# Kernel optimization log

Measured on AMD Instinct MI355X. Metric: run time of the kernel, lower is better.

## Reference

```python
import jax, jax.numpy as jnp
import numpy as np
from jax.scipy.special import logsumexp

# Circuit configuration (matches init_kwargs)
V, K, C = 256, 32, 256        # num_vars, input nodes per var, num categories
N = V * K                     # nodes per layer (8192)
E, PF, SF, L = 32768, 4, 16, 5  # elements/layer, prod fan-in, sum fan-in, layer pairs
B = 512                       # batch size


def setup_inputs() -> dict:
    key = jax.random.key(0)
    k0, k1, k2, k3, k4, k5 = jax.random.split(key, 6)
    inputs = jax.random.randint(k0, (B, V), 0, C)                     # [B, num_vars]
    input_logps = jax.nn.log_softmax(jax.random.normal(k1, (V, K, C)), axis=-1)
    prod_children = jax.random.randint(k2, (L, E, PF), 0, N)          # element -> child nodes
    sum_children = jax.random.randint(k3, (L, N, SF), 0, E)           # sum node -> child elements
    sum_logw = jax.nn.log_softmax(jax.random.normal(k4, (L, N, SF)), axis=-1)
    root_logw = jax.nn.log_softmax(jax.random.normal(k5, (N,)))
    return {"inputs": inputs, "input_logps": input_logps,
            "prod_children": prod_children, "sum_children": sum_children,
            "sum_logw": sum_logw, "root_logw": root_logw}


def reference(inputs, input_logps, prod_children, sum_children, sum_logw, root_logw):
    V_, K_, C_ = input_logps.shape
    B_ = inputs.shape[0]
    N_ = V_ * K_

    # ---- input layer: node_mars[v*K+k, b] = log p_{v,k}(inputs[b, v]) ----
    idx = jnp.broadcast_to(inputs.T[:, None, :], (V_, K_, B_))        # [V, K, B]
    node_mars = jnp.take_along_axis(input_logps, idx, axis=2)         # [V, K, B]
    node_mars = node_mars.reshape(N_, B_)                             # [num_nodes, B]

    # ---- inner layers: alternating product (segment log-sum) / sum (logsumexp) ----
    def layer(nm, xs):
        pc, sc, lw = xs                                               # [E,PF], [N,SF], [N,SF]
        element_mars = nm[pc].sum(axis=1)                             # prod: [E, PF, B] -> [E, B]
        nm_next = logsumexp(element_mars[sc] + lw[..., None], axis=1) # sum:  [N, SF, B] -> [N, B]
        return nm_next, None

    node_mars, _ = jax.lax.scan(layer, node_mars, (prod_children, sum_children, sum_logw))
    # ---- root sum node over all last-layer nodes ----
    lls = logsumexp(node_mars + root_logw[:, None], axis=0)           # [B]
    return lls[:, None]                                               # [B, num_roots=1]
```

## Files before the change

### kernel.cpp

```cpp
#include <hip/hip_runtime.h>
#include <hip/hip_fp16.h>

namespace {

constexpr int V_ = 256, K_ = 32, C_ = 256;
constexpr int N_ = V_ * K_;
constexpr int E_ = 32768, PF_ = 4, SF_ = 16, L_ = 5;
constexpr int B_ = 512;
constexpr int NCH = 64;
constexpr int NSLICE = B_ / 8;
constexpr int NCHK = 4;
constexpr int NPB = N_ / NCHK;

constexpr float LOG2E = 1.4426950408889634f;
constexpr float LN2   = 0.6931471805599453f;

typedef _Float16 h2v __attribute__((ext_vector_type(2)));

__device__ __forceinline__ uint32_t f2h(float a, float b) {
    __half2 h = __floats2half2_rn(a, b);
    return *reinterpret_cast<uint32_t*>(&h);
}
__device__ __forceinline__ h2v splat2h(uint32_t bits) {
    const _Float16 h = __builtin_bit_cast(_Float16, (unsigned short)(bits & 0xffffu));
    h2v r; r.x = h; r.y = h; return r;
}
__device__ __forceinline__ float2 h2f2(h2v v) {
    return make_float2((float)v.x, (float)v.y);
}
__device__ __forceinline__ h2v u2h(uint32_t u) { return __builtin_bit_cast(h2v, u); }

__global__ void prep_k(const int* __restrict__ sc,
                       const int* __restrict__ pc,
                       const float* __restrict__ lw,
                       ushort4* __restrict__ pcx,
                       __half* __restrict__ lwh)
{
    const int t = blockIdx.x * blockDim.x + threadIdx.x;
    const int l = t >> 17;
    const int e = sc[t];
    const int4 p = *reinterpret_cast<const int4*>(pc + ((size_t)l * E_ + e) * 4);
    ushort4 u;
    u.x = (unsigned short)p.x; u.y = (unsigned short)p.y;
    u.z = (unsigned short)p.z; u.w = (unsigned short)p.w;
    pcx[t] = u;
    lwh[t] = __float2half(lw[t] * LOG2E);
}

__global__ void input_layer_k(const int* __restrict__ inp,
                              const float* __restrict__ lp,
                              uint4* __restrict__ nm)
{
    const int t = blockIdx.x * blockDim.x + threadIdx.x;
    const int vk = t & (N_ - 1);
    const int bs = t >> 13;
    const int v = vk >> 5;
    const int b = bs * 8;
    const float* row = lp + (size_t)vk * C_;
    uint4 r;
    r.x = f2h(row[inp[(b + 0) * V_ + v]] * LOG2E, row[inp[(b + 1) * V_ + v]] * LOG2E);
    r.y = f2h(row[inp[(b + 2) * V_ + v]] * LOG2E, row[inp[(b + 3) * V_ + v]] * LOG2E);
    r.z = f2h(row[inp[(b + 4) * V_ + v]] * LOG2E, row[inp[(b + 5) * V_ + v]] * LOG2E);
    r.w = f2h(row[inp[(b + 6) * V_ + v]] * LOG2E, row[inp[(b + 7) * V_ + v]] * LOG2E);
    nm[(size_t)bs * N_ + vk] = r;
}

__global__ __launch_bounds__(1024, 4) void layer_k(
    const uint4* __restrict__ nmi,
    const uint4* __restrict__ pcx,
    const uint4* __restrict__ lwh,
    uint4* __restrict__ nmo)
{
    __shared__ uint4 lds[N_];
    const int bs = blockIdx.x & (NSLICE - 1);
    const int nc = blockIdx.x >> 6;

    const uint4* src = nmi + (size_t)bs * N_;
    for (int i = threadIdx.x; i < N_; i += 1024) lds[i] = src[i];
    __syncthreads();

    #pragma unroll
    for (int r = 0; r < 2; ++r) {
        const int n = nc * NPB + r * 1024 + threadIdx.x;
        const uint4* pr = pcx + (size_t)n * 8;
        const uint4* wr = lwh + (size_t)n * 2;

        h2v xs[8][4], m2[4], cm[4];
        float acc[8];

        auto children8 = [&](const uint4 pw0, const uint4 pw1, const uint4 pw2,
                             const uint4 pw3, const uint4 wv) {
            auto child = [&](int s8, uint32_t rr0, uint32_t rr1, uint32_t wbits) {
                const uint4 a = lds[rr0 & 0xffffu];
                const uint4 b = lds[rr0 >> 16];
                const uint4 c = lds[rr1 & 0xffffu];
                const uint4 d = lds[rr1 >> 16];
                const h2v w2 = splat2h(wbits);
                #pragma unroll
                for (int q = 0; q < 4; ++q) {
                    h2v t = (u2h((&a.x)[q]) + u2h((&b.x)[q]))
                          + (u2h((&c.x)[q]) + u2h((&d.x)[q]));
                    t = t + w2;
                    xs[s8][q] = t;
                    cm[q] = __builtin_elementwise_max(cm[q], t);
                }
            };
            child(0, pw0.x, pw0.y, wv.x);
            child(1, pw0.z, pw0.w, wv.x >> 16);
            child(2, pw1.x, pw1.y, wv.y);
            child(3, pw1.z, pw1.w, wv.y >> 16);
            child(4, pw2.x, pw2.y, wv.z);
            child(5, pw2.z, pw2.w, wv.z >> 16);
            child(6, pw3.x, pw3.y, wv.w);
            child(7, pw3.z, pw3.w, wv.w >> 16);
        };

        #pragma unroll
        for (int q = 0; q < 4; ++q) cm[q] = splat2h(0xF7FFu);
        #pragma unroll
        for (int q = 0; q < 4; ++q) cm[q] = splat2h(0xF400u);
        children8(pr[0], pr[1], pr[2], pr[3], wr[0]);
        #pragma unroll
        for (int q = 0; q < 4; ++q) m2[q] = cm[q];
        #pragma unroll
        for (int j = 0; j < 8; ++j) acc[j] = 0.f;
        #pragma unroll
        for (int s = 0; s < 8; ++s) {
            #pragma unroll
            for (int q = 0; q < 4; ++q) {
                const float2 f = h2f2(xs[s][q] - m2[q]);
                acc[2 * q + 0] += exp2f(f.x);
                acc[2 * q + 1] += exp2f(f.y);
            }
        }

        #pragma unroll
        for (int q = 0; q < 4; ++q) cm[q] = splat2h(0xF400u);
        children8(pr[4], pr[5], pr[6], pr[7], wr[1]);
        #pragma unroll
        for (int q = 0; q < 4; ++q) {
            const h2v mm = __builtin_elementwise_max(m2[q], cm[q]);
            const float2 df = h2f2(m2[q] - mm);
            acc[2 * q + 0] *= exp2f(df.x);
            acc[2 * q + 1] *= exp2f(df.y);
            m2[q] = mm;
        }
        #pragma unroll
        for (int s = 0; s < 8; ++s) {
            #pragma unroll
            for (int q = 0; q < 4; ++q) {
                const float2 f = h2f2(xs[s][q] - m2[q]);
                acc[2 * q + 0] += exp2f(f.x);
                acc[2 * q + 1] += exp2f(f.y);
            }
        }

        uint4 o;
        {
            const float2 f0 = h2f2(m2[0]);
            const float2 f1 = h2f2(m2[1]);
            o.x = f2h(f0.x + log2f(acc[0]), f0.y + log2f(acc[1]));
            o.y = f2h(f1.x + log2f(acc[2]), f1.y + log2f(acc[3]));
        }
        {
            const float2 f2v = h2f2(m2[2]);
            const float2 f3v = h2f2(m2[3]);
            o.z = f2h(f2v.x + log2f(acc[4]), f2v.y + log2f(acc[5]));
            o.w = f2h(f3v.x + log2f(acc[6]), f3v.y + log2f(acc[7]));
        }
        nmo[(size_t)bs * N_ + n] = o;
    }
}

__global__ void root_part_k(const __half* __restrict__ nm,
                            const float* __restrict__ rw,
                            float* __restrict__ pm,
                            float* __restrict__ ps)
{
    const int b = blockIdx.x * blockDim.x + threadIdx.x;
    const int ch = blockIdx.y;
    const int n0 = ch * (N_ / NCH);
    const int bs = b >> 3, j = b & 7;
    float m = -3.0e38f, s = 0.f;
    for (int i = 0; i < N_ / NCH; ++i) {
        const int n = n0 + i;
        const float x = __half2float(nm[((size_t)bs * N_ + n) * 8 + j]) + rw[n] * LOG2E;
        const float mn = fmaxf(m, x);
        s = s * exp2f(m - mn) + exp2f(x - mn);
        m = mn;
    }
    pm[ch * B_ + b] = m;
    ps[ch * B_ + b] = s;
}

__global__ void root_comb_k(const float* __restrict__ pm,
                            const float* __restrict__ ps,
                            float* __restrict__ out)
{
    const int b = blockIdx.x * blockDim.x + threadIdx.x;
    float m = -3.0e38f;
    for (int ch = 0; ch < NCH; ++ch) m = fmaxf(m, pm[ch * B_ + b]);
    float s = 0.f;
    for (int ch = 0; ch < NCH; ++ch) s += ps[ch * B_ + b] * exp2f(pm[ch * B_ + b] - m);
    out[b] = (m + log2f(s)) * LN2;
}

}

extern "C" void kernel_launch(void* const* d_in, const int* in_sizes, int n_in,
                              void* d_out, int out_size, void* d_ws, size_t ws_size,
                              hipStream_t stream) {
    const int*   inp = (const int*)d_in[0];
    const float* lp  = (const float*)d_in[1];
    const int*   pc  = (const int*)d_in[2];
    const int*   sc  = (const int*)d_in[3];
    const float* lw  = (const float*)d_in[4];
    const float* rw  = (const float*)d_in[5];
    float*       out = (float*)d_out;

    uint4*   nm0 = (uint4*)d_ws;
    uint4*   nm1 = nm0 + (size_t)NSLICE * N_;
    ushort4* pcx = (ushort4*)(nm1 + (size_t)NSLICE * N_);
    __half*  lwh = (__half*)(pcx + (size_t)L_ * N_ * SF_);
    float*   pm  = (float*)(lwh + (size_t)L_ * N_ * SF_);
    float*   ps  = pm + (size_t)NCH * B_;

    prep_k<<<(L_ * N_ * SF_) / 256, 256, 0, stream>>>(sc, pc, lw, pcx, lwh);
    input_layer_k<<<(NSLICE * N_) / 256, 256, 0, stream>>>(inp, lp, nm0);

    for (int l = 0; l < L_; ++l) {
        const uint4* srcb = (l & 1) ? nm1 : nm0;
        uint4*       dstb = (l & 1) ? nm0 : nm1;
        layer_k<<<NSLICE * NCHK, 1024, 0, stream>>>(
            srcb,
            (const uint4*)(pcx + (size_t)l * N_ * SF_),
            (const uint4*)(lwh + (size_t)l * N_ * SF_),
            dstb);
    }
    const uint4* fin = (L_ & 1) ? nm1 : nm0;

    root_part_k<<<dim3(B_ / 256, NCH), 256, 0, stream>>>((const __half*)fin, rw, pm, ps);
    root_comb_k<<<B_ / 256, 256, 0, stream>>>(pm, ps, out);
}
```

Before: 163.0 us.

## Fuse root reduction into last layer and merge prep with input layer

Merges the prep and input-layer kernels into one setup launch. Folds the root log-weights into the last layer's sum weights so the root logsumexp happens inside that layer. The last layer reduces over its nodes with wave shuffles and LDS, and writes per-chunk partial max/sum pairs, which removes the final node_mars write and the root_part_k pass. The root weight is now added in fp16 before the exp, which may shift precision slightly.

Result: slower. 260.2 us (+59.6%).

```diff
diff --git a/kernel.cpp b/kernel.cpp
--- a/kernel.cpp
+++ b/kernel.cpp
@@ -7,11 +7,13 @@
 constexpr int N_ = V_ * K_;
 constexpr int E_ = 32768, PF_ = 4, SF_ = 16, L_ = 5;
 constexpr int B_ = 512;
-constexpr int NCH = 64;
 constexpr int NSLICE = B_ / 8;
 constexpr int NCHK = 4;
 constexpr int NPB = N_ / NCHK;
 
+constexpr int PREP_T  = L_ * N_ * SF_;
+constexpr int INPUT_T = NSLICE * N_;
+
 constexpr float LOG2E = 1.4426950408889634f;
 constexpr float LN2   = 0.6931471805599453f;
 
@@ -30,39 +32,114 @@
 }
 __device__ __forceinline__ h2v u2h(uint32_t u) { return __builtin_bit_cast(h2v, u); }
 
-__global__ void prep_k(const int* __restrict__ sc,
-                       const int* __restrict__ pc,
-                       const float* __restrict__ lw,
-                       ushort4* __restrict__ pcx,
-                       __half* __restrict__ lwh)
+__global__ void setup_k(const int* __restrict__ sc,
+                        const int* __restrict__ pc,
+                        const float* __restrict__ lw,
+                        const float* __restrict__ rw,
+                        const int* __restrict__ inp,
+                        const float* __restrict__ lp,
+                        ushort4* __restrict__ pcx,
+                        __half* __restrict__ lwh,
+                        uint4* __restrict__ nm)
 {
     const int t = blockIdx.x * blockDim.x + threadIdx.x;
-    const int l = t >> 17;
-    const int e = sc[t];
-    const int4 p = *reinterpret_cast<const int4*>(pc + ((size_t)l * E_ + e) * 4);
-    ushort4 u;
-    u.x = (unsigned short)p.x; u.y = (unsigned short)p.y;
-    u.z = (unsigned short)p.z; u.w = (unsigned short)p.w;
-    pcx[t] = u;
-    lwh[t] = __float2half(lw[t] * LOG2E);
-}
-
-__global__ void input_layer_k(const int* __restrict__ inp,
-                              const float* __restrict__ lp,
-                              uint4* __restrict__ nm)
-{
-    const int t = blockIdx.x * blockDim.x + threadIdx.x;
-    const int vk = t & (N_ - 1);
-    const int bs = t >> 13;
-    const int v = vk >> 5;
-    const int b = bs * 8;
-    const float* row = lp + (size_t)vk * C_;
-    uint4 r;
-    r.x = f2h(row[inp[(b + 0) * V_ + v]] * LOG2E, row[inp[(b + 1) * V_ + v]] * LOG2E);
-    r.y = f2h(row[inp[(b + 2) * V_ + v]] * LOG2E, row[inp[(b + 3) * V_ + v]] * LOG2E);
-    r.z = f2h(row[inp[(b + 4) * V_ + v]] * LOG2E, row[inp[(b + 5) * V_ + v]] * LOG2E);
-    r.w = f2h(row[inp[(b + 6) * V_ + v]] * LOG2E, row[inp[(b + 7) * V_ + v]] * LOG2E);
-    nm[(size_t)bs * N_ + vk] = r;
+    if (t < PREP_T) {
+        const int l = t >> 17;
+        const int n = (t >> 4) & (N_ - 1);
+        const int e = sc[t];
+        const int4 p = *reinterpret_cast<const int4*>(pc + ((size_t)l * E_ + e) * 4);
+        ushort4 u;
+        u.x = (unsigned short)p.x; u.y = (unsigned short)p.y;
+        u.z = (unsigned short)p.z; u.w = (unsigned short)p.w;
+        pcx[t] = u;
+        const float add = (l == L_ - 1) ? rw[n] : 0.f;
+        lwh[t] = __float2half((lw[t] + add) * LOG2E);
+    } else {
+        const int t2 = t - PREP_T;
+        const int vk = t2 & (N_ - 1);
+        const int bs = t2 >> 13;
+        const int v = vk >> 5;
+        const int b = bs * 8;
+        const float* row = lp + (size_t)vk * C_;
+        uint4 r;
+        r.x = f2h(row[inp[(b + 0) * V_ + v]] * LOG2E, row[inp[(b + 1) * V_ + v]] * LOG2E);
+        r.y = f2h(row[inp[(b + 2) * V_ + v]] * LOG2E, row[inp[(b + 3) * V_ + v]] * LOG2E);
+        r.z = f2h(row[inp[(b + 4) * V_ + v]] * LOG2E, row[inp[(b + 5) * V_ + v]] * LOG2E);
+        r.w = f2h(row[inp[(b + 6) * V_ + v]] * LOG2E, row[inp[(b + 7) * V_ + v]] * LOG2E);
+        nm[(size_t)bs * N_ + vk] = r;
+    }
+}
+
+template <typename LDS>
+__device__ __forceinline__ void node_lse(const LDS& lds, const uint4* pr, const uint4* wr,
+                                         h2v m2[4], float acc[8])
+{
+    h2v xs[8][4], cm[4];
+
+    auto children8 = [&](const uint4 pw0, const uint4 pw1, const uint4 pw2,
+                         const uint4 pw3, const uint4 wv) {
+        auto child = [&](int s8, uint32_t rr0, uint32_t rr1, uint32_t wbits) {
+            const uint4 a = lds[rr0 & 0xffffu];
+            const uint4 b = lds[rr0 >> 16];
+            const uint4 c = lds[rr1 & 0xffffu];
+            const uint4 d = lds[rr1 >> 16];
+            const h2v w2 = splat2h(wbits);
+            #pragma unroll
+            for (int q = 0; q < 4; ++q) {
+                h2v t = (u2h((&a.x)[q]) + u2h((&b.x)[q]))
+                      + (u2h((&c.x)[q]) + u2h((&d.x)[q]));
+                t = t + w2;
+                xs[s8][q] = t;
+                cm[q] = __builtin_elementwise_max(cm[q], t);
+            }
+        };
+        child(0, pw0.x, pw0.y, wv.x);
+        child(1, pw0.z, pw0.w, wv.x >> 16);
+        child(2, pw1.x, pw1.y, wv.y);
+        child(3, pw1.z, pw1.w, wv.y >> 16);
+        child(4, pw2.x, pw2.y, wv.z);
+        child(5, pw2.z, pw2.w, wv.z >> 16);
+        child(6, pw3.x, pw3.y, wv.w);
+        child(7, pw3.z, pw3.w, wv.w >> 16);
+    };
+
+    #pragma unroll
+    for (int q = 0; q < 4; ++q) cm[q] = splat2h(0xF400u);
+    children8(pr[0], pr[1], pr[2], pr[3], wr[0]);
+    #pragma unroll
+    for (int q = 0; q < 4; ++q) m2[q] = cm[q];
+    #pragma unroll
+    for (int j = 0; j < 8; ++j) acc[j] = 0.f;
+    #pragma unroll
+    for (int s = 0; s < 8; ++s) {
+        #pragma unroll
+        for (int q = 0; q < 4; ++q) {
+            const float2 f = h2f2(xs[s][q] - m2[q]);
+            acc[2 * q + 0] += exp2f(f.x);
+            acc[2 * q + 1] += exp2f(f.y);
+        }
+    }
+
+    #pragma unroll
+    for (int q = 0; q < 4; ++q) cm[q] = splat2h(0xF400u);
+    children8(pr[4], pr[5], pr[6], pr[7], wr[1]);
+    #pragma unroll
+    for (int q = 0; q < 4; ++q) {
+        const h2v mm = __builtin_elementwise_max(m2[q], cm[q]);
+        const float2 df = h2f2(m2[q] - mm);
+        acc[2 * q + 0] *= exp2f(df.x);
+        acc[2 * q + 1] *= exp2f(df.y);
+        m2[q] = mm;
+    }
+    #pragma unroll
+    for (int s = 0; s < 8; ++s) {
+        #pragma unroll
+        for (int q = 0; q < 4; ++q) {
+            const float2 f = h2f2(xs[s][q] - m2[q]);
+            acc[2 * q + 0] += exp2f(f.x);
+            acc[2 * q + 1] += exp2f(f.y);
+        }
+    }
 }
 
 __global__ __launch_bounds__(1024, 4) void layer_k(
@@ -82,78 +159,9 @@
     #pragma unroll
     for (int r = 0; r < 2; ++r) {
         const int n = nc * NPB + r * 1024 + threadIdx.x;
-        const uint4* pr = pcx + (size_t)n * 8;
-        const uint4* wr = lwh + (size_t)n * 2;
-
-        h2v xs[8][4], m2[4], cm[4];
+        h2v m2[4];
         float acc[8];
-
-        auto children8 = [&](const uint4 pw0, const uint4 pw1, const uint4 pw2,
-                             const uint4 pw3, const uint4 wv) {
-            auto child = [&](int s8, uint32_t rr0, uint32_t rr1, uint32_t wbits) {
-                const uint4 a = lds[rr0 & 0xffffu];
-                const uint4 b = lds[rr0 >> 16];
-                const uint4 c = lds[rr1 & 0xffffu];
-                const uint4 d = lds[rr1 >> 16];
-                const h2v w2 = splat2h(wbits);
-                #pragma unroll
-                for (int q = 0; q < 4; ++q) {
-                    h2v t = (u2h((&a.x)[q]) + u2h((&b.x)[q]))
-                          + (u2h((&c.x)[q]) + u2h((&d.x)[q]));
-                    t = t + w2;
-                    xs[s8][q] = t;
-                    cm[q] = __builtin_elementwise_max(cm[q], t);
-                }
-            };
-            child(0, pw0.x, pw0.y, wv.x);
-            child(1, pw0.z, pw0.w, wv.x >> 16);
-            child(2, pw1.x, pw1.y, wv.y);
-            child(3, pw1.z, pw1.w, wv.y >> 16);
-            child(4, pw2.x, pw2.y, wv.z);
-            child(5, pw2.z, pw2.w, wv.z >> 16);
-            child(6, pw3.x, pw3.y, wv.w);
-            child(7, pw3.z, pw3.w, wv.w >> 16);
-        };
-
-        #pragma unroll
-        for (int q = 0; q < 4; ++q) cm[q] = splat2h(0xF7FFu);
-        #pragma unroll
-        for (int q = 0; q < 4; ++q) cm[q] = splat2h(0xF400u);
-        children8(pr[0], pr[1], pr[2], pr[3], wr[0]);
-        #pragma unroll
-        for (int q = 0; q < 4; ++q) m2[q] = cm[q];
-        #pragma unroll
-        for (int j = 0; j < 8; ++j) acc[j] = 0.f;
-        #pragma unroll
-        for (int s = 0; s < 8; ++s) {
-            #pragma unroll
-            for (int q = 0; q < 4; ++q) {
-                const float2 f = h2f2(xs[s][q] - m2[q]);
-                acc[2 * q + 0] += exp2f(f.x);
-                acc[2 * q + 1] += exp2f(f.y);
-            }
-        }
-
-        #pragma unroll
-        for (int q = 0; q < 4; ++q) cm[q] = splat2h(0xF400u);
-        children8(pr[4], pr[5], pr[6], pr[7], wr[1]);
-        #pragma unroll
-        for (int q = 0; q < 4; ++q) {
-            const h2v mm = __builtin_elementwise_max(m2[q], cm[q]);
-            const float2 df = h2f2(m2[q] - mm);
-            acc[2 * q + 0] *= exp2f(df.x);
-            acc[2 * q + 1] *= exp2f(df.y);
-            m2[q] = mm;
-        }
-        #pragma unroll
-        for (int s = 0; s < 8; ++s) {
-            #pragma unroll
-            for (int q = 0; q < 4; ++q) {
-                const float2 f = h2f2(xs[s][q] - m2[q]);
-                acc[2 * q + 0] += exp2f(f.x);
-                acc[2 * q + 1] += exp2f(f.y);
-            }
-        }
+        node_lse(lds, pcx + (size_t)n * 8, lwh + (size_t)n * 2, m2, acc);
 
         uint4 o;
         {
@@ -172,25 +180,84 @@
     }
 }
 
-__global__ void root_part_k(const __half* __restrict__ nm,
-                            const float* __restrict__ rw,
-                            float* __restrict__ pm,
-                            float* __restrict__ ps)
-{
-    const int b = blockIdx.x * blockDim.x + threadIdx.x;
-    const int ch = blockIdx.y;
-    const int n0 = ch * (N_ / NCH);
-    const int bs = b >> 3, j = b & 7;
-    float m = -3.0e38f, s = 0.f;
-    for (int i = 0; i < N_ / NCH; ++i) {
-        const int n = n0 + i;
-        const float x = __half2float(nm[((size_t)bs * N_ + n) * 8 + j]) + rw[n] * LOG2E;
-        const float mn = fmaxf(m, x);
-        s = s * exp2f(m - mn) + exp2f(x - mn);
-        m = mn;
-    }
-    pm[ch * B_ + b] = m;
-    ps[ch * B_ + b] = s;
+__global__ __launch_bounds__(1024, 4) void layer_last_k(
+    const uint4* __restrict__ nmi,
+    const uint4* __restrict__ pcx,
+    const uint4* __restrict__ lwh,
+    float* __restrict__ pm,
+    float* __restrict__ ps)
+{
+    __shared__ uint4 lds[N_];
+    const int bs = blockIdx.x & (NSLICE - 1);
+    const int nc = blockIdx.x >> 6;
+
+    const uint4* src = nmi + (size_t)bs * N_;
+    for (int i = threadIdx.x; i < N_; i += 1024) lds[i] = src[i];
+    __syncthreads();
+
+    float rm[8], rs[8];
+    #pragma unroll
+    for (int j = 0; j < 8; ++j) { rm[j] = -3.0e38f; rs[j] = 0.f; }
+
+    #pragma unroll
+    for (int r = 0; r < 2; ++r) {
+        const int n = nc * NPB + r * 1024 + threadIdx.x;
+        h2v m2[4];
+        float acc[8];
+        node_lse(lds, pcx + (size_t)n * 8, lwh + (size_t)n * 2, m2, acc);
+
+        #pragma unroll
+        for (int q = 0; q < 4; ++q) {
+            const float2 f = h2f2(m2[q]);
+            {
+                const float nmax = fmaxf(rm[2 * q], f.x);
+                rs[2 * q] = rs[2 * q] * exp2f(rm[2 * q] - nmax) + acc[2 * q] * exp2f(f.x - nmax);
+                rm[2 * q] = nmax;
+            }
+            {
+                const float nmax = fmaxf(rm[2 * q + 1], f.y);
+                rs[2 * q + 1] = rs[2 * q + 1] * exp2f(rm[2 * q + 1] - nmax)
+                              + acc[2 * q + 1] * exp2f(f.y - nmax);
+                rm[2 * q + 1] = nmax;
+            }
+        }
+    }
+
+    for (int d = 1; d < 64; d <<= 1) {
+        #pragma unroll
+        for (int j = 0; j < 8; ++j) {
+            const float om = __shfl_xor(rm[j], d);
+            const float os = __shfl_xor(rs[j], d);
+            const float nmax = fmaxf(rm[j], om);
+            rs[j] = rs[j] * exp2f(rm[j] - nmax) + os * exp2f(om - nmax);
+            rm[j] = nmax;
+        }
+    }
+
+    __syncthreads();
+    float* red = reinterpret_cast<float*>(lds);
+    const int wid = threadIdx.x >> 6;
+    if ((threadIdx.x & 63) == 0) {
+        #pragma unroll
+        for (int j = 0; j < 8; ++j) {
+            red[(wid * 8 + j) * 2 + 0] = rm[j];
+            red[(wid * 8 + j) * 2 + 1] = rs[j];
+        }
+    }
+    __syncthreads();
+    if (threadIdx.x < 8) {
+        const int j = threadIdx.x;
+        float M = -3.0e38f, S = 0.f;
+        for (int w = 0; w < 16; ++w) {
+            const float m_ = red[(w * 8 + j) * 2 + 0];
+            const float s_ = red[(w * 8 + j) * 2 + 1];
+            const float nmax = fmaxf(M, m_);
+            S = S * exp2f(M - nmax) + s_ * exp2f(m_ - nmax);
+            M = nmax;
+        }
+        pm[nc * B_ + bs * 8 + j] = M;
+        ps[nc * B_ + bs * 8 + j] = S;
+    }
 }
 
 __global__ void root_comb_k(const float* __restrict__ pm,
@@ -198,11 +265,15 @@
                             float* __restrict__ out)
 {
     const int b = blockIdx.x * blockDim.x + threadIdx.x;
-    float m = -3.0e38f;
-    for (int ch = 0; ch < NCH; ++ch) m = fmaxf(m, pm[ch * B_ + b]);
-    float s = 0.f;
-    for (int ch = 0; ch < NCH; ++ch) s += ps[ch * B_ + b] * exp2f(pm[ch * B_ + b] - m);
-    out[b] = (m + log2f(s)) * LN2;
+    float M = -3.0e38f, S = 0.f;
+    for (int c = 0; c < NCHK; ++c) {
+        const float m_ = pm[c * B_ + b];
+        const float s_ = ps[c * B_ + b];
+        const float nmax = fmaxf(M, m_);
+        S = S * exp2f(M - nmax) + s_ * exp2f(m_ - nmax);
+        M = nmax;
+    }
+    out[b] = (M + log2f(S)) * LN2;
 }
 
 }
@@ -223,12 +294,12 @@
     ushort4* pcx = (ushort4*)(nm1 + (size_t)NSLICE * N_);
     __half*  lwh = (__half*)(pcx + (size_t)L_ * N_ * SF_);
     float*   pm  = (float*)(lwh + (size_t)L_ * N_ * SF_);
-    float*   ps  = pm + (size_t)NCH * B_;
-
-    prep_k<<<(L_ * N_ * SF_) / 256, 256, 0, stream>>>(sc, pc, lw, pcx, lwh);
-    input_layer_k<<<(NSLICE * N_) / 256, 256, 0, stream>>>(inp, lp, nm0);
-
-    for (int l = 0; l < L_; ++l) {
+    float*   ps  = pm + (size_t)NCHK * B_;
+
+    setup_k<<<(PREP_T + INPUT_T) / 256, 256, 0, stream>>>(
+        sc, pc, lw, rw, inp, lp, pcx, lwh, nm0);
+
+    for (int l = 0; l < L_ - 1; ++l) {
         const uint4* srcb = (l & 1) ? nm1 : nm0;
         uint4*       dstb = (l & 1) ? nm0 : nm1;
         layer_k<<<NSLICE * NCHK, 1024, 0, stream>>>(
@@ -237,8 +308,11 @@
             (const uint4*)(lwh + (size_t)l * N_ * SF_),
             dstb);
     }
-    const uint4* fin = (L_ & 1) ? nm1 : nm0;
-
-    root_part_k<<<dim3(B_ / 256, NCH), 256, 0, stream>>>((const __half*)fin, rw, pm, ps);
+    layer_last_k<<<NSLICE * NCHK, 1024, 0, stream>>>(
+        nm0,
+        (const uint4*)(pcx + (size_t)(L_ - 1) * N_ * SF_),
+        (const uint4*)(lwh + (size_t)(L_ - 1) * N_ * SF_),
+        pm, ps);
+
     root_comb_k<<<B_ / 256, 256, 0, stream>>>(pm, ps, out);
 }
```
